# Kernel tuning notes

Measured on AMD Instinct MI355X. Metric: run time of the kernel, lower is better.

The kernel has to match this reference:

```python
import jax, jax.numpy as jnp
import numpy as np

N, C, H, W = 32, 24, 14, 14
HD, GH, AS = 128, 256, 28
D_IN = (C + 2) * 2 + HD  # 180


def setup_inputs() -> dict:
    key = jax.random.key(0)
    ks = jax.random.split(key, 10)
    s = 0.05
    inp = {
        "x": jax.random.normal(ks[0], (N, C, H, W), jnp.float32),
        "code": jax.random.normal(ks[1], (N, HD), jnp.float32),
        "gw0": jax.random.normal(ks[2], (D_IN, GH), jnp.float32) * s,
        "gb0": jnp.zeros((GH,), jnp.float32),
        "gw1": jax.random.normal(ks[3], (GH, GH), jnp.float32) * s,
        "gb1": jnp.zeros((GH,), jnp.float32),
        "gw2": jax.random.normal(ks[4], (GH, GH), jnp.float32) * s,
        "gb2": jnp.zeros((GH,), jnp.float32),
        "gw3": jax.random.normal(ks[5], (GH, GH), jnp.float32) * s,
        "gb3": jnp.zeros((GH,), jnp.float32),
        "fw0": jax.random.normal(ks[6], (GH, GH), jnp.float32) * s,
        "fb0": jnp.zeros((GH,), jnp.float32),
        "fw1": jax.random.normal(ks[7], (GH, GH), jnp.float32) * s,
        "fb1": jnp.zeros((GH,), jnp.float32),
        "fw2": jax.random.normal(ks[8], (GH, AS), jnp.float32) * s,
        "fb2": jnp.zeros((AS,), jnp.float32),
    }
    return inp


def _rn_encode(x, code):
    n, c, h, w = x.shape
    o = h * w
    hd = code.shape[1]
    # coordinates: torch.linspace(-h/2, h/2, h) over row dim, (-w/2, w/2, w) over col dim
    xs = jnp.linspace(-h / 2.0, h / 2.0, h, dtype=jnp.float32)
    ys = jnp.linspace(-w / 2.0, w / 2.0, w, dtype=jnp.float32)
    coord = jnp.stack(
        [jnp.broadcast_to(xs[:, None], (h, w)).reshape(o),
         jnp.broadcast_to(ys[None, :], (h, w)).reshape(o)], axis=-1)  # (o, 2)
    feats = x.reshape(n, c, o).transpose(0, 2, 1)  # (n, o, c)
    feats = jnp.concatenate([feats, jnp.broadcast_to(coord, (n, o, 2))], axis=-1)  # (n, o, c+2)
    # pairs[n, i, j] = [feats[n, j], feats[n, i], code[n]]  (matches torch expand semantics)
    p1 = jnp.broadcast_to(feats[:, None, :, :], (n, o, o, c + 2))
    p2 = jnp.broadcast_to(feats[:, :, None, :], (n, o, o, c + 2))
    q = jnp.broadcast_to(code[:, None, None, :], (n, o, o, hd))
    return jnp.concatenate([p1, p2, q], axis=-1).reshape(n, o * o, -1)


def reference(x, code, gw0, gb0, gw1, gb1, gw2, gb2, gw3, gb3,
              fw0, fb0, fw1, fb1, fw2, fb2):
    pairs = _rn_encode(x, code)  # (n, o^2, 180)
    h1 = jax.nn.relu(pairs @ gw0 + gb0)
    h1 = jax.nn.relu(h1 @ gw1 + gb1)
    h1 = jax.nn.relu(h1 @ gw2 + gb2)
    h1 = jax.nn.relu(h1 @ gw3 + gb3)
    relations = h1.sum(axis=1)  # (n, GH) sum-pool over all pairs
    r = jax.nn.relu(relations @ fw0 + fb0)
    r = jax.nn.relu(r @ fw1 + fb1)
    logits = r @ fw2 + fb2  # last layer linear (last=True)
    return logits
```

## Files before the change

### kernel.cpp

```cpp
#include <hip/hip_runtime.h>
#include <hip/hip_bf16.h>


typedef __attribute__((ext_vector_type(8))) short short8;
typedef __attribute__((ext_vector_type(16))) float f32x16;

#define NIMG 32
#define O 196
#define PAIRS 38416
#define GH 256
#define AS 28
#define ROWS 96
#define CHUNKS 401

#define SWZ(row) ((((row) & 7) << 4) ^ (((row) & 8) << 2))

static __device__ __forceinline__ unsigned short f2bf(float f) {
    __hip_bfloat16 h = __float2bfloat16(f);
    return *reinterpret_cast<unsigned short*>(&h);
}

__global__ void k_cc(const float* __restrict__ code, const float* __restrict__ gw0,
                     const float* __restrict__ gb0, float* __restrict__ CC) {
    const int n = blockIdx.x, g = threadIdx.x;
    __shared__ float cs[128];
    if (g < 128) cs[g] = code[n * 128 + g];
    __syncthreads();
    float acc = gb0[g];
    for (int k = 0; k < 128; ++k) acc = fmaf(cs[k], gw0[(52 + k) * GH + g], acc);
    CC[n * GH + g] = acc;
}

__global__ void k_ajbi(const float* __restrict__ x, const float* __restrict__ gw0,
                       const float* __restrict__ CC,
                       float* __restrict__ AJ, float* __restrict__ BI) {
    const int np = blockIdx.x;
    const int n = np / O, p = np - n * O;
    const int g = threadIdx.x;
    __shared__ float fs[26];
    if (g < 24)       fs[g]  = x[(n * 24 + g) * O + p];
    else if (g == 24) fs[24] = -7.0f + (float)(p / 14) * (14.0f / 13.0f);
    else if (g == 25) fs[25] = -7.0f + (float)(p % 14) * (14.0f / 13.0f);
    __syncthreads();
    float aj = CC[n * GH + g], bi = 0.f;
#pragma unroll
    for (int c = 0; c < 26; ++c) {
        const float f = fs[c];
        aj = fmaf(f, gw0[c * GH + g], aj);
        bi = fmaf(f, gw0[(26 + c) * GH + g], bi);
    }
    AJ[np * GH + g] = aj;
    BI[np * GH + g] = bi;
}

__global__ void k_pack(const float* __restrict__ gw1, const float* __restrict__ gw2,
                       const float* __restrict__ gw3, unsigned short* __restrict__ pW) {
    const int idx = blockIdx.x * 256 + threadIdx.x;
    const int L = idx >> 16;
    const int rem = idx & 0xFFFF;
    const int e = rem & 7;
    const int lane = (rem >> 3) & 63;
    const int ks = (rem >> 9) & 15;
    const int nt = rem >> 13;
    const int k = ks * 16 + ((lane >> 5) << 3) + e;
    const int col = nt * 32 + (lane & 31);
    const float* W = (L == 0) ? gw1 : (L == 1) ? gw2 : gw3;
    pW[idx] = f2bf(W[k * GH + col]);
}

__global__ __launch_bounds__(512, 4) void k_main(
    const float* __restrict__ AJ, const float* __restrict__ BI,
    const unsigned short* __restrict__ pW,
    const float* __restrict__ gb1, const float* __restrict__ gb2,
    const float* __restrict__ gb3, float* __restrict__ rel) {
    __shared__ __attribute__((aligned(16))) unsigned short h[ROWS * GH];

    const int blk = blockIdx.x;
    const int n = blk / CHUNKS;
    const int chunk = blk - n * CHUNKS;
    const int row_base = chunk * ROWS;
    const int t = threadIdx.x;
    const int wave = t >> 6;
    const int lane = t & 63;
    const int l31 = lane & 31;
    const int hi = lane >> 5;
    const int l15 = lane & 15;
    const bool tail = (chunk == CHUNKS - 1);

    {
        const int i0 = row_base / O;
        const int j00 = row_base - i0 * O;
        const int i1 = min(i0 + 1, O - 1);
        const float4 bi0 = *(const float4*)&BI[(n * O + i0) * GH + lane * 4];
        const float4 bi1 = *(const float4*)&BI[(n * O + i1) * GH + lane * 4];
#pragma unroll
        for (int e = 0; e < 12; ++e) {
            const int r = wave + e * 8;
            const int jj = j00 + r;
            const bool wrap = (jj >= O);
            const int j = wrap ? jj - O : jj;
            const float4 aj = *(const float4*)&AJ[(n * O + j) * GH + lane * 4];
            const float4 bi = wrap ? bi1 : bi0;
            const unsigned int lo = (unsigned)f2bf(fmaxf(aj.x + bi.x, 0.f)) |
                                    ((unsigned)f2bf(fmaxf(aj.y + bi.y, 0.f)) << 16);
            const unsigned int hh = (unsigned)f2bf(fmaxf(aj.z + bi.z, 0.f)) |
                                    ((unsigned)f2bf(fmaxf(aj.w + bi.w, 0.f)) << 16);
            const int byteoff = r * 512 + ((lane * 8) ^ SWZ(r));
            uint2 dd; dd.x = lo; dd.y = hh;
            *(uint2*)((char*)h + byteoff) = dd;
        }
    }
    __syncthreads();

    const float* gbs[3] = {gb1, gb2, gb3};
    const int X = SWZ(l15);
    const int arow = l31 * 512;
    const int hi16 = hi << 4;
    const char* hB = (const char*)h;

    for (int layer = 0; layer < 3; ++layer) {
        f32x16 acc0 = {0.f,0.f,0.f,0.f,0.f,0.f,0.f,0.f,0.f,0.f,0.f,0.f,0.f,0.f,0.f,0.f};
        f32x16 acc1 = acc0, acc2 = acc0;

        const short8* wp = (const short8*)(pW + layer * 65536 + wave * 8192);
        short8 b0 = wp[0 * 64 + lane];
        short8 b1 = wp[1 * 64 + lane];
#pragma unroll
        for (int ks = 0; ks < 16; ++ks) {
            const short8 b = b0;
            b0 = b1;
            if (ks < 14) b1 = wp[(ks + 2) * 64 + lane];
            const int off = (ks * 32 + hi16) ^ X;
            const short8 a0 = *(const short8*)(hB + arow + off);
            const short8 a1 = *(const short8*)(hB + arow + off + 16384);
            const short8 a2 = *(const short8*)(hB + arow + off + 32768);
            acc0 = __builtin_amdgcn_mfma_f32_32x32x16_bf16(a0, b, acc0, 0, 0, 0);
            acc1 = __builtin_amdgcn_mfma_f32_32x32x16_bf16(a1, b, acc1, 0, 0, 0);
            acc2 = __builtin_amdgcn_mfma_f32_32x32x16_bf16(a2, b, acc2, 0, 0, 0);
        }
        __syncthreads();

        const float bias = gbs[layer][wave * 32 + l31];
        if (layer < 2) {
            const int colb = (wave * 32 + l31) * 2;
#pragma unroll
            for (int r = 0; r < 16; ++r) {
                const int rr = (r & 3) + 8 * (r >> 2) + 4 * hi;
                const int swz = colb ^ SWZ(rr);
                *(unsigned short*)((char*)h + (rr      ) * 512 + swz) =
                    f2bf(fmaxf(acc0[r] + bias, 0.0f));
                *(unsigned short*)((char*)h + (rr +  32) * 512 + swz) =
                    f2bf(fmaxf(acc1[r] + bias, 0.0f));
                *(unsigned short*)((char*)h + (rr +  64) * 512 + swz) =
                    f2bf(fmaxf(acc2[r] + bias, 0.0f));
            }
            __syncthreads();
        } else {
            float s = 0.f;
            if (!tail) {
#pragma unroll
                for (int r = 0; r < 16; ++r)
                    s += fmaxf(acc0[r] + bias, 0.0f) +
                         fmaxf(acc1[r] + bias, 0.0f) +
                         fmaxf(acc2[r] + bias, 0.0f);
            } else {
#pragma unroll
                for (int r = 0; r < 8; ++r)
                    s += fmaxf(acc0[r] + bias, 0.0f);
            }
            s += __shfl_xor(s, 32);
            if (hi == 0) atomicAdd(&rel[n * GH + wave * 32 + l31], s);
        }
    }
}

__global__ void k_fmlp(const float* __restrict__ rel,
                       const float* __restrict__ fw0, const float* __restrict__ fb0,
                       const float* __restrict__ fw1, const float* __restrict__ fb1,
                       const float* __restrict__ fw2, const float* __restrict__ fb2,
                       float* __restrict__ out) {
    __shared__ float b0[GH], b1[GH];
    const int n = blockIdx.x, g = threadIdx.x;
    b0[g] = rel[n * GH + g];
    __syncthreads();
    float a = fb0[g];
    for (int k = 0; k < GH; ++k) a = fmaf(b0[k], fw0[k * GH + g], a);
    b1[g] = fmaxf(a, 0.f);
    __syncthreads();
    float c = fb1[g];
    for (int k = 0; k < GH; ++k) c = fmaf(b1[k], fw1[k * GH + g], c);
    b0[g] = fmaxf(c, 0.f);
    __syncthreads();
    if (g < AS) {
        float o = fb2[g];
        for (int k = 0; k < GH; ++k) o = fmaf(b0[k], fw2[k * AS + g], o);
        out[n * AS + g] = o;
    }
}

extern "C" void kernel_launch(void* const* d_in, const int* in_sizes, int n_in,
                              void* d_out, int out_size, void* d_ws, size_t ws_size,
                              hipStream_t stream) {
    const float* x    = (const float*)d_in[0];
    const float* code = (const float*)d_in[1];
    const float* gw0  = (const float*)d_in[2];
    const float* gb0  = (const float*)d_in[3];
    const float* gw1  = (const float*)d_in[4];
    const float* gb1  = (const float*)d_in[5];
    const float* gw2  = (const float*)d_in[6];
    const float* gb2  = (const float*)d_in[7];
    const float* gw3  = (const float*)d_in[8];
    const float* gb3  = (const float*)d_in[9];
    const float* fw0  = (const float*)d_in[10];
    const float* fb0  = (const float*)d_in[11];
    const float* fw1  = (const float*)d_in[12];
    const float* fb1  = (const float*)d_in[13];
    const float* fw2  = (const float*)d_in[14];
    const float* fb2  = (const float*)d_in[15];
    float* out = (float*)d_out;

    char* ws = (char*)d_ws;
    float*          AJ  = (float*)(ws + 0);
    float*          BI  = (float*)(ws + 6422528);
    float*          CC  = (float*)(ws + 12845056);
    float*          rel = (float*)(ws + 12877824);
    unsigned short* pW  = (unsigned short*)(ws + 12910592);

    hipMemsetAsync(rel, 0, NIMG * GH * sizeof(float), stream);
    k_cc<<<NIMG, 256, 0, stream>>>(code, gw0, gb0, CC);
    k_ajbi<<<NIMG * O, 256, 0, stream>>>(x, gw0, CC, AJ, BI);
    k_pack<<<768, 256, 0, stream>>>(gw1, gw2, gw3, pW);
    k_main<<<NIMG * CHUNKS, 512, 0, stream>>>(AJ, BI, pW, gb1, gb2, gb3, rel);
    k_fmlp<<<NIMG, 256, 0, stream>>>(rel, fw0, fb0, fw1, fb1, fw2, fb2, out);
}
```

Baseline: 563.7 us.

## Enlarge pair chunk to 128 rows and use 2x2 MFMA warp tiles

Measured after the change: 584.4 us. 3.7% more time.

```diff
diff --git a/kernel.cpp b/kernel.cpp
--- a/kernel.cpp
+++ b/kernel.cpp
@@ -10,8 +10,8 @@
 #define PAIRS 38416
 #define GH 256
 #define AS 28
-#define ROWS 96
-#define CHUNKS 401
+#define ROWS 128
+#define CHUNKS 301
 
 #define SWZ(row) ((((row) & 7) << 4) ^ (((row) & 8) << 2))
 
@@ -85,6 +85,8 @@
     const int l31 = lane & 31;
     const int hi = lane >> 5;
     const int l15 = lane & 15;
+    const int mq = wave >> 2;
+    const int nq = wave & 3;
     const bool tail = (chunk == CHUNKS - 1);
 
     {
@@ -94,7 +96,7 @@
         const float4 bi0 = *(const float4*)&BI[(n * O + i0) * GH + lane * 4];
         const float4 bi1 = *(const float4*)&BI[(n * O + i1) * GH + lane * 4];
 #pragma unroll
-        for (int e = 0; e < 12; ++e) {
+        for (int e = 0; e < 16; ++e) {
             const int r = wave + e * 8;
             const int jj = j00 + r;
             const bool wrap = (jj >= O);
@@ -114,62 +116,77 @@
 
     const float* gbs[3] = {gb1, gb2, gb3};
     const int X = SWZ(l15);
-    const int arow = l31 * 512;
+    const int arow = (mq * 64 + l31) * 512;
     const int hi16 = hi << 4;
     const char* hB = (const char*)h;
 
     for (int layer = 0; layer < 3; ++layer) {
-        f32x16 acc0 = {0.f,0.f,0.f,0.f,0.f,0.f,0.f,0.f,0.f,0.f,0.f,0.f,0.f,0.f,0.f,0.f};
-        f32x16 acc1 = acc0, acc2 = acc0;
-
-        const short8* wp = (const short8*)(pW + layer * 65536 + wave * 8192);
-        short8 b0 = wp[0 * 64 + lane];
-        short8 b1 = wp[1 * 64 + lane];
+        f32x16 acc00 = {0.f,0.f,0.f,0.f,0.f,0.f,0.f,0.f,0.f,0.f,0.f,0.f,0.f,0.f,0.f,0.f};
+        f32x16 acc01 = acc00, acc10 = acc00, acc11 = acc00;
+
+        const short8* wp0 = (const short8*)(pW + layer * 65536 + (nq * 2) * 8192);
+        const short8* wp1 = wp0 + 1024;
+        short8 p00 = wp0[lane],      p10 = wp1[lane];
+        short8 p01 = wp0[64 + lane], p11 = wp1[64 + lane];
 #pragma unroll
         for (int ks = 0; ks < 16; ++ks) {
-            const short8 b = b0;
-            b0 = b1;
-            if (ks < 14) b1 = wp[(ks + 2) * 64 + lane];
+            const short8 b0 = p00, b1 = p10;
+            p00 = p01; p10 = p11;
+            if (ks < 14) {
+                p01 = wp0[(ks + 2) * 64 + lane];
+                p11 = wp1[(ks + 2) * 64 + lane];
+            }
             const int off = (ks * 32 + hi16) ^ X;
             const short8 a0 = *(const short8*)(hB + arow + off);
             const short8 a1 = *(const short8*)(hB + arow + off + 16384);
-            const short8 a2 = *(const short8*)(hB + arow + off + 32768);
-            acc0 = __builtin_amdgcn_mfma_f32_32x32x16_bf16(a0, b, acc0, 0, 0, 0);
-            acc1 = __builtin_amdgcn_mfma_f32_32x32x16_bf16(a1, b, acc1, 0, 0, 0);
-            acc2 = __builtin_amdgcn_mfma_f32_32x32x16_bf16(a2, b, acc2, 0, 0, 0);
+            acc00 = __builtin_amdgcn_mfma_f32_32x32x16_bf16(a0, b0, acc00, 0, 0, 0);
+            acc01 = __builtin_amdgcn_mfma_f32_32x32x16_bf16(a0, b1, acc01, 0, 0, 0);
+            acc10 = __builtin_amdgcn_mfma_f32_32x32x16_bf16(a1, b0, acc10, 0, 0, 0);
+            acc11 = __builtin_amdgcn_mfma_f32_32x32x16_bf16(a1, b1, acc11, 0, 0, 0);
         }
         __syncthreads();
 
-        const float bias = gbs[layer][wave * 32 + l31];
+        const float bias0 = gbs[layer][nq * 64 + l31];
+        const float bias1 = gbs[layer][nq * 64 + 32 + l31];
         if (layer < 2) {
-            const int colb = (wave * 32 + l31) * 2;
+            const int colb0 = (nq * 64 + l31) * 2;
 #pragma unroll
             for (int r = 0; r < 16; ++r) {
                 const int rr = (r & 3) + 8 * (r >> 2) + 4 * hi;
-                const int swz = colb ^ SWZ(rr);
-                *(unsigned short*)((char*)h + (rr      ) * 512 + swz) =
-                    f2bf(fmaxf(acc0[r] + bias, 0.0f));
-                *(unsigned short*)((char*)h + (rr +  32) * 512 + swz) =
-                    f2bf(fmaxf(acc1[r] + bias, 0.0f));
-                *(unsigned short*)((char*)h + (rr +  64) * 512 + swz) =
-                    f2bf(fmaxf(acc2[r] + bias, 0.0f));
+                const int rb0 = (mq * 64 + rr) * 512;
+                const int s0 = colb0 ^ SWZ(rr);
+                const int s1 = (colb0 + 64) ^ SWZ(rr);
+                *(unsigned short*)((char*)h + rb0 + s0) =
+                    f2bf(fmaxf(acc00[r] + bias0, 0.0f));
+                *(unsigned short*)((char*)h + rb0 + s1) =
+                    f2bf(fmaxf(acc01[r] + bias1, 0.0f));
+                *(unsigned short*)((char*)h + rb0 + 16384 + s0) =
+                    f2bf(fmaxf(acc10[r] + bias0, 0.0f));
+                *(unsigned short*)((char*)h + rb0 + 16384 + s1) =
+                    f2bf(fmaxf(acc11[r] + bias1, 0.0f));
             }
             __syncthreads();
         } else {
-            float s = 0.f;
+            float s0 = 0.f, s1 = 0.f;
             if (!tail) {
 #pragma unroll
-                for (int r = 0; r < 16; ++r)
-                    s += fmaxf(acc0[r] + bias, 0.0f) +
-                         fmaxf(acc1[r] + bias, 0.0f) +
-                         fmaxf(acc2[r] + bias, 0.0f);
-            } else {
-#pragma unroll
-                for (int r = 0; r < 8; ++r)
-                    s += fmaxf(acc0[r] + bias, 0.0f);
-            }
-            s += __shfl_xor(s, 32);
-            if (hi == 0) atomicAdd(&rel[n * GH + wave * 32 + l31], s);
+                for (int r = 0; r < 16; ++r) {
+                    s0 += fmaxf(acc00[r] + bias0, 0.0f) + fmaxf(acc10[r] + bias0, 0.0f);
+                    s1 += fmaxf(acc01[r] + bias1, 0.0f) + fmaxf(acc11[r] + bias1, 0.0f);
+                }
+            } else if (mq == 0) {
+#pragma unroll
+                for (int r = 0; r < 8; ++r) {
+                    s0 += fmaxf(acc00[r] + bias0, 0.0f);
+                    s1 += fmaxf(acc01[r] + bias1, 0.0f);
+                }
+            }
+            s0 += __shfl_xor(s0, 32);
+            s1 += __shfl_xor(s1, 32);
+            if (hi == 0) {
+                atomicAdd(&rel[n * GH + nq * 64 + l31], s0);
+                atomicAdd(&rel[n * GH + nq * 64 + 32 + l31], s1);
+            }
         }
     }
 }
```

## Double-buffer LDS activations with transposed MFMA to drop a barrier per layer

Applied to the files above, without the earlier changes.

New measurement: 593.2 us. 5.2% more time.

```diff
diff --git a/kernel.cpp b/kernel.cpp
--- a/kernel.cpp
+++ b/kernel.cpp
@@ -10,8 +10,8 @@
 #define PAIRS 38416
 #define GH 256
 #define AS 28
-#define ROWS 96
-#define CHUNKS 401
+#define ROWS 64
+#define CHUNKS 601
 
 #define SWZ(row) ((((row) & 7) << 4) ^ (((row) & 8) << 2))
 
@@ -73,7 +73,8 @@
     const unsigned short* __restrict__ pW,
     const float* __restrict__ gb1, const float* __restrict__ gb2,
     const float* __restrict__ gb3, float* __restrict__ rel) {
-    __shared__ __attribute__((aligned(16))) unsigned short h[ROWS * GH];
+    __shared__ __attribute__((aligned(16))) unsigned short hA[ROWS * GH];
+    __shared__ __attribute__((aligned(16))) unsigned short hB[ROWS * GH];
 
     const int blk = blockIdx.x;
     const int n = blk / CHUNKS;
@@ -94,7 +95,7 @@
         const float4 bi0 = *(const float4*)&BI[(n * O + i0) * GH + lane * 4];
         const float4 bi1 = *(const float4*)&BI[(n * O + i1) * GH + lane * 4];
 #pragma unroll
-        for (int e = 0; e < 12; ++e) {
+        for (int e = 0; e < 8; ++e) {
             const int r = wave + e * 8;
             const int jj = j00 + r;
             const bool wrap = (jj >= O);
@@ -107,70 +108,95 @@
                                     ((unsigned)f2bf(fmaxf(aj.w + bi.w, 0.f)) << 16);
             const int byteoff = r * 512 + ((lane * 8) ^ SWZ(r));
             uint2 dd; dd.x = lo; dd.y = hh;
-            *(uint2*)((char*)h + byteoff) = dd;
-        }
-    }
-    __syncthreads();
-
-    const float* gbs[3] = {gb1, gb2, gb3};
+            *(uint2*)((char*)hA + byteoff) = dd;
+        }
+    }
+    __syncthreads();
+
     const int X = SWZ(l15);
+    const int hi16 = hi << 4;
     const int arow = l31 * 512;
-    const int hi16 = hi << 4;
-    const char* hB = (const char*)h;
-
-    for (int layer = 0; layer < 3; ++layer) {
-        f32x16 acc0 = {0.f,0.f,0.f,0.f,0.f,0.f,0.f,0.f,0.f,0.f,0.f,0.f,0.f,0.f,0.f,0.f};
-        f32x16 acc1 = acc0, acc2 = acc0;
-
-        const short8* wp = (const short8*)(pW + layer * 65536 + wave * 8192);
-        short8 b0 = wp[0 * 64 + lane];
-        short8 b1 = wp[1 * 64 + lane];
+
+    auto kloop = [&](const unsigned short* bufR, const short8* wp,
+                     f32x16& a0, f32x16& a1, bool swapped) {
+        short8 wa = wp[lane], wb = wp[64 + lane], wc = wp[128 + lane], wd = wp[192 + lane];
+        const char* hb = (const char*)bufR + arow;
 #pragma unroll
         for (int ks = 0; ks < 16; ++ks) {
-            const short8 b = b0;
-            b0 = b1;
-            if (ks < 14) b1 = wp[(ks + 2) * 64 + lane];
+            const short8 W = (ks & 3) == 0 ? wa : (ks & 3) == 1 ? wb
+                           : (ks & 3) == 2 ? wc : wd;
             const int off = (ks * 32 + hi16) ^ X;
-            const short8 a0 = *(const short8*)(hB + arow + off);
-            const short8 a1 = *(const short8*)(hB + arow + off + 16384);
-            const short8 a2 = *(const short8*)(hB + arow + off + 32768);
-            acc0 = __builtin_amdgcn_mfma_f32_32x32x16_bf16(a0, b, acc0, 0, 0, 0);
-            acc1 = __builtin_amdgcn_mfma_f32_32x32x16_bf16(a1, b, acc1, 0, 0, 0);
-            acc2 = __builtin_amdgcn_mfma_f32_32x32x16_bf16(a2, b, acc2, 0, 0, 0);
-        }
-        __syncthreads();
-
-        const float bias = gbs[layer][wave * 32 + l31];
-        if (layer < 2) {
-            const int colb = (wave * 32 + l31) * 2;
-#pragma unroll
-            for (int r = 0; r < 16; ++r) {
-                const int rr = (r & 3) + 8 * (r >> 2) + 4 * hi;
-                const int swz = colb ^ SWZ(rr);
-                *(unsigned short*)((char*)h + (rr      ) * 512 + swz) =
-                    f2bf(fmaxf(acc0[r] + bias, 0.0f));
-                *(unsigned short*)((char*)h + (rr +  32) * 512 + swz) =
-                    f2bf(fmaxf(acc1[r] + bias, 0.0f));
-                *(unsigned short*)((char*)h + (rr +  64) * 512 + swz) =
-                    f2bf(fmaxf(acc2[r] + bias, 0.0f));
+            const short8 h0 = *(const short8*)(hb + off);
+            const short8 h1 = *(const short8*)(hb + off + 16384);
+            if (swapped) {
+                a0 = __builtin_amdgcn_mfma_f32_32x32x16_bf16(W, h0, a0, 0, 0, 0);
+                a1 = __builtin_amdgcn_mfma_f32_32x32x16_bf16(W, h1, a1, 0, 0, 0);
+            } else {
+                a0 = __builtin_amdgcn_mfma_f32_32x32x16_bf16(h0, W, a0, 0, 0, 0);
+                a1 = __builtin_amdgcn_mfma_f32_32x32x16_bf16(h1, W, a1, 0, 0, 0);
             }
-            __syncthreads();
+            if (ks < 12) {
+                const short8 nw = wp[(ks + 4) * 64 + lane];
+                if ((ks & 3) == 0) wa = nw; else if ((ks & 3) == 1) wb = nw;
+                else if ((ks & 3) == 2) wc = nw; else wd = nw;
+            }
+        }
+    };
+
+    auto epi = [&](const f32x16& a0, const f32x16& a1, const float* gb,
+                   unsigned short* bufW) {
+        const float4 b40 = *(const float4*)&gb[wave * 32 + 0  + 4 * hi];
+        const float4 b41 = *(const float4*)&gb[wave * 32 + 8  + 4 * hi];
+        const float4 b42 = *(const float4*)&gb[wave * 32 + 16 + 4 * hi];
+        const float4 b43 = *(const float4*)&gb[wave * 32 + 24 + 4 * hi];
+        const float bias[16] = {b40.x, b40.y, b40.z, b40.w, b41.x, b41.y, b41.z, b41.w,
+                                b42.x, b42.y, b42.z, b42.w, b43.x, b43.y, b43.z, b43.w};
+        char* w0 = (char*)bufW + l31 * 512;
+#pragma unroll
+        for (int rp = 0; rp < 8; ++rp) {
+            const int r0 = rp * 2;
+            const float ba = bias[(r0 >> 2) * 4 + (r0 & 3)];
+            const float bb = bias[(r0 >> 2) * 4 + (r0 & 3) + 1];
+            const int cw = (r0 & 3) + 8 * (r0 >> 2);
+            const int cb = (wave * 64 + cw * 2 + hi * 8) ^ X;
+            const unsigned p0 = (unsigned)f2bf(fmaxf(a0[r0] + ba, 0.f)) |
+                                ((unsigned)f2bf(fmaxf(a0[r0 + 1] + bb, 0.f)) << 16);
+            const unsigned p1 = (unsigned)f2bf(fmaxf(a1[r0] + ba, 0.f)) |
+                                ((unsigned)f2bf(fmaxf(a1[r0 + 1] + bb, 0.f)) << 16);
+            *(unsigned*)(w0 + cb) = p0;
+            *(unsigned*)(w0 + 16384 + cb) = p1;
+        }
+    };
+
+    const f32x16 z = {0.f,0.f,0.f,0.f,0.f,0.f,0.f,0.f,0.f,0.f,0.f,0.f,0.f,0.f,0.f,0.f};
+    const short8* wpb = (const short8*)pW + wave * 1024;
+
+    f32x16 acc0 = z, acc1 = z;
+    kloop(hA, wpb, acc0, acc1, true);
+    epi(acc0, acc1, gb1, hB);
+    __syncthreads();
+
+    acc0 = z; acc1 = z;
+    kloop(hB, wpb + 8192, acc0, acc1, true);
+    epi(acc0, acc1, gb2, hA);
+    __syncthreads();
+
+    acc0 = z; acc1 = z;
+    kloop(hA, wpb + 16384, acc0, acc1, false);
+    {
+        const float bias = gb3[wave * 32 + l31];
+        float s = 0.f;
+        if (!tail) {
+#pragma unroll
+            for (int r = 0; r < 16; ++r)
+                s += fmaxf(acc0[r] + bias, 0.f) + fmaxf(acc1[r] + bias, 0.f);
         } else {
-            float s = 0.f;
-            if (!tail) {
-#pragma unroll
-                for (int r = 0; r < 16; ++r)
-                    s += fmaxf(acc0[r] + bias, 0.0f) +
-                         fmaxf(acc1[r] + bias, 0.0f) +
-                         fmaxf(acc2[r] + bias, 0.0f);
-            } else {
-#pragma unroll
-                for (int r = 0; r < 8; ++r)
-                    s += fmaxf(acc0[r] + bias, 0.0f);
-            }
-            s += __shfl_xor(s, 32);
-            if (hi == 0) atomicAdd(&rel[n * GH + wave * 32 + l31], s);
-        }
+#pragma unroll
+            for (int r = 0; r < 8; ++r)
+                s += fmaxf(acc0[r] + bias, 0.f);
+        }
+        s += __shfl_xor(s, 32);
+        if (hi == 0) atomicAdd(&rel[n * GH + wave * 32 + l31], s);
     }
 }
 
```
